# Performance work log

Hardware: AMD Instinct MI355X
Metric: run time of the kernel (lower is better)

## Reference

```python
import jax, jax.numpy as jnp
import numpy as np

B, QS, KS, E, H = 2, 2048, 2048, 2048, 16
D = E // H  # head_dim = 128
EPS = 1e-6


def setup_inputs() -> dict:
    key = jax.random.key(0)
    ks = jax.random.split(key, 11)
    scale_in = 1.0 / np.sqrt(E)  # lecun_normal fan_in = E
    scale_out = 1.0 / np.sqrt(E)  # fan_in for out proj = H*D = E
    return {
        "q": jax.random.normal(ks[0], (B, QS, E), jnp.float32),
        "kv": jax.random.normal(ks[1], (B, KS, E), jnp.float32),
        "q_pos": jax.random.normal(ks[2], (B, QS, E), jnp.float32),
        "kv_pos": jax.random.normal(ks[3], (B, KS, E), jnp.float32),
        "mask": jax.random.bernoulli(ks[4], 0.5, (B, QS, KS)),
        "wq": jax.random.normal(ks[5], (E, H, D), jnp.float32) * scale_in,
        "wk": jax.random.normal(ks[6], (E, H, D), jnp.float32) * scale_in,
        "wv": jax.random.normal(ks[7], (E, H, D), jnp.float32) * scale_in,
        "q_ln_scale": jnp.ones((D,), jnp.float32),
        "k_ln_scale": jnp.ones((D,), jnp.float32),
        "wo": jax.random.normal(ks[8], (H, D, E), jnp.float32) * scale_out,
    }


def _layernorm_no_bias(x, scale):
    # flax LayerNorm over last axis, use_bias=False, epsilon=1e-6
    mu = jnp.mean(x, axis=-1, keepdims=True)
    var = jnp.mean(jnp.square(x - mu), axis=-1, keepdims=True)
    return (x - mu) * jax.lax.rsqrt(var + EPS) * scale


def reference(q, kv, q_pos, kv_pos, mask, wq, wk, wv, q_ln_scale, k_ln_scale, wo):
    dtype = q.dtype
    qi = q + q_pos          # [b, qs, e]
    ki = kv + kv_pos        # [b, ks, e]
    vi = kv
    # QKV projections (DenseGeneral, no bias) -> [b, s, h, d]
    qh = jnp.einsum('bqe,ehd->bqhd', qi, wq)
    kh = jnp.einsum('bke,ehd->bkhd', ki, wk)
    vh = jnp.einsum('bke,ehd->bkhd', vi, wv)
    # normalize_qk: LayerNorm (no bias) on query/key over head_dim
    qh = _layernorm_no_bias(qh, q_ln_scale)
    kh = _layernorm_no_bias(kh, k_ln_scale)
    # scaled dot-product with float32 logits
    qh = qh / jnp.sqrt(jnp.asarray(D, dtype))
    logits = jnp.einsum('bqhd,bkhd->bhqk', qh, kh,
                        preferred_element_type=jnp.float32)
    big_neg = jnp.finfo(jnp.float32).min
    logits = jnp.where(mask[:, None, :, :], logits, big_neg)
    attn = jax.nn.softmax(logits, axis=-1).astype(dtype)  # [b,h,q,k]
    out = jnp.einsum('bhqk,bkhd->bqhd', attn, vh)
    # output projection (DenseGeneral over (h,d), no bias)
    return jnp.einsum('bqhd,hde->bqe', out, wo)
```

## Files before the change

### kernel.cpp

```cpp
#include <hip/hip_runtime.h>
#include <hip/hip_bf16.h>


typedef __attribute__((ext_vector_type(8))) __bf16 bf16x8;
typedef __attribute__((ext_vector_type(4))) float f32x4;
typedef __attribute__((ext_vector_type(16))) float f32x16;
typedef __attribute__((ext_vector_type(8))) unsigned short ushort8;
typedef __attribute__((ext_vector_type(4))) unsigned short ushort4v;
typedef __attribute__((ext_vector_type(4))) unsigned uint4v;
typedef __attribute__((ext_vector_type(4))) float float4v;

#define MFMA16(a, b, c) __builtin_amdgcn_mfma_f32_16x16x32_bf16((a), (b), (c), 0, 0, 0)
#define MFMA32(a, b, c) __builtin_amdgcn_mfma_f32_32x32x16_bf16((a), (b), (c), 0, 0, 0)

__device__ __forceinline__ unsigned short f2bf(float f) {
  unsigned u = __builtin_bit_cast(unsigned, f);
  u += 0x7fffu + ((u >> 16) & 1u);
  return (unsigned short)(u >> 16);
}

__device__ __forceinline__ unsigned pkbf(float lo, float hi) {
  unsigned d;
  asm("v_cvt_pk_bf16_f32 %0, %1, %2" : "=v"(d) : "v"(lo), "v"(hi));
  return d;
}

__device__ __forceinline__ float max3f(float a, float b, float c) {
  float d;
  asm("v_max3_f32 %0, %1, %2, %3" : "=v"(d) : "v"(a), "v"(b), "v"(c));
  return d;
}

__device__ __forceinline__ float exp2a(float x) {
  float d;
  asm("v_exp_f32 %0, %1" : "=v"(d) : "v"(x));
  return d;
}

__device__ __forceinline__ void gload_lds16(const void* g, void* l) {
  __builtin_amdgcn_global_load_lds(
      (const __attribute__((address_space(1))) void*)g,
      (__attribute__((address_space(3))) void*)l, 16, 0, 0);
}

__global__ __launch_bounds__(256) void k_prep(const float4v* __restrict__ q,
                                              const float4v* __restrict__ q_pos,
                                              const float4v* __restrict__ kv,
                                              const float4v* __restrict__ kv_pos,
                                              const int* __restrict__ mask,
                                              ushort4v* __restrict__ a_q,
                                              ushort4v* __restrict__ a_k,
                                              ushort4v* __restrict__ a_v,
                                              unsigned long long* __restrict__ mkb,
                                              const float* __restrict__ s0, const float* __restrict__ s1,
                                              const float* __restrict__ s2, const float* __restrict__ s3,
                                              unsigned short* __restrict__ d0, unsigned short* __restrict__ d1,
                                              unsigned short* __restrict__ d2, unsigned short* __restrict__ d3) {
  __shared__ float t[32][33];
  int bx = blockIdx.x, tid = threadIdx.x;
  if (bx < 8192) {
    int i = bx * 256 + tid;
    float4v a = q[i] + q_pos[i];
    ushort4v r;
    r[0] = f2bf(a[0]); r[1] = f2bf(a[1]); r[2] = f2bf(a[2]); r[3] = f2bf(a[3]);
    a_q[i] = r;
  } else if (bx < 16384) {
    int i = (bx - 8192) * 256 + tid;
    float4v a = kv[i];
    float4v s = a + kv_pos[i];
    ushort4v ra, rb;
    ra[0] = f2bf(s[0]); ra[1] = f2bf(s[1]); ra[2] = f2bf(s[2]); ra[3] = f2bf(s[3]);
    rb[0] = f2bf(a[0]); rb[1] = f2bf(a[1]); rb[2] = f2bf(a[2]); rb[3] = f2bf(a[3]);
    a_k[i] = ra; a_v[i] = rb;
  } else if (bx < 49152) {
    int i = (bx - 16384) * 256 + tid;
    unsigned long long b = __ballot(mask[i] != 0);
    if ((tid & 63) == 0) mkb[i >> 6] = b;
  } else {
    int idx = bx - 49152;
    int z = idx >> 12, rem = idx & 4095;
    int r0 = (rem >> 6) * 32, c0 = (rem & 63) * 32;
    const float* S; unsigned short* D;
    switch (z) {
      case 0: S = s0; D = d0; break;
      case 1: S = s1; D = d1; break;
      case 2: S = s2; D = d2; break;
      default: S = s3; D = d3; break;
    }
    int x = tid & 31, y = tid >> 5;
#pragma unroll
    for (int i = 0; i < 4; ++i) t[y + 8 * i][x] = S[(size_t)(r0 + y + 8 * i) * 2048 + c0 + x];
    __syncthreads();
#pragma unroll
    for (int i = 0; i < 4; ++i)
      D[(size_t)(c0 + y + 8 * i) * 2048 + r0 + x] = f2bf(t[x][y + 8 * i]);
  }
}

template <int MODE>
__global__ __launch_bounds__(512, 2) void k_gemm8(const unsigned short* __restrict__ A,
                                                  const unsigned short* __restrict__ Bt,
                                                  void* __restrict__ Cv,
                                                  const float* __restrict__ lnsc) {
  constexpr int K = 2048;
  constexpr int NT = 32;
  constexpr int BUF = 49152;
  __shared__ __attribute__((aligned(16))) char smem[3 * BUF];
  int tid = threadIdx.x;
  int lane = tid & 63, w = tid >> 6;
  int wr = w >> 2, wc = w & 3;
  int r15 = lane & 15, blk = lane >> 4;
  int L = blockIdx.y * gridDim.x + blockIdx.x;
  int xcd = L & 7, slot = L >> 3;
  int mt, nt;
  if constexpr (MODE == 4) { mt = xcd; nt = slot; }
  else { mt = xcd * 2 + (slot >> 4); nt = slot & 15; }
  int n0 = nt * 128, m0 = mt * 256;
  const unsigned short* Abase = A + (size_t)m0 * K;
  const unsigned short* Bbase = Bt + (size_t)n0 * K;
  f32x4 acc[8][2] = {};

  const unsigned short* ag[4]; int al[4];
  const unsigned short* bg[2]; int bl[2];
#pragma unroll
  for (int i = 0; i < 4; ++i) {
    int c = i * 512 + tid;
    int row = c >> 3, cc = c & 7;
    ag[i] = Abase + (size_t)row * K + ((cc ^ (row & 7)) * 8);
    al[i] = c * 16;
  }
#pragma unroll
  for (int i = 0; i < 2; ++i) {
    int c = i * 512 + tid;
    int row = c >> 3, cc = c & 7;
    bg[i] = Bbase + (size_t)row * K + ((cc ^ (row & 7)) * 8);
    bl[i] = 32768 + c * 16;
  }

  auto stage = [&](int t) {
    char* buf = smem + (t % 3) * BUF;
    int kt = t * 64;
#pragma unroll
    for (int i = 0; i < 4; ++i) gload_lds16(ag[i] + kt, buf + al[i]);
#pragma unroll
    for (int i = 0; i < 2; ++i) gload_lds16(bg[i] + kt, buf + bl[i]);
  };

  stage(0);
  stage(1);

  for (int t = 0; t < NT; ++t) {
    if (t + 2 < NT) {
      stage(t + 2);
      asm volatile("s_waitcnt vmcnt(12)" ::: "memory");
    } else if (t + 1 < NT) {
      asm volatile("s_waitcnt vmcnt(6)" ::: "memory");
    } else {
      asm volatile("s_waitcnt vmcnt(0)" ::: "memory");
    }
    __builtin_amdgcn_s_barrier();
    __builtin_amdgcn_sched_barrier(0);
    const unsigned short* sA = (const unsigned short*)(smem + (t % 3) * BUF);
    const unsigned short* sB = (const unsigned short*)(smem + (t % 3) * BUF + 32768);
#pragma unroll
    for (int kk = 0; kk < 2; ++kk) {
      bf16x8 av[8], bv[2];
#pragma unroll
      for (int i = 0; i < 8; ++i) {
        int row = wr * 128 + i * 16 + r15;
        av[i] = *(const bf16x8*)&sA[row * 64 + (((kk * 4 + blk) ^ (row & 7)) * 8)];
      }
#pragma unroll
      for (int j = 0; j < 2; ++j) {
        int row = wc * 32 + j * 16 + r15;
        bv[j] = *(const bf16x8*)&sB[row * 64 + (((kk * 4 + blk) ^ (row & 7)) * 8)];
      }
#pragma unroll
      for (int i = 0; i < 8; ++i)
#pragma unroll
        for (int j = 0; j < 2; ++j) acc[i][j] = MFMA16(av[i], bv[j], acc[i][j]);
    }
    asm volatile("s_waitcnt lgkmcnt(0)" ::: "memory");
    __builtin_amdgcn_s_barrier();
  }
  __syncthreads();

  if constexpr (MODE == 3) {
    float* C = (float*)Cv;
#pragma unroll
    for (int i = 0; i < 8; ++i)
#pragma unroll
      for (int r = 0; r < 4; ++r) {
        int rowl = wr * 128 + i * 16 + blk * 4 + r;
#pragma unroll
        for (int j = 0; j < 2; ++j) {
          int coll = wc * 32 + j * 16 + r15;
          C[(size_t)(m0 + rowl) * 2048 + n0 + coll] = acc[i][j][r];
        }
      }
  } else if constexpr (MODE == 4) {
    unsigned short* Vtp = (unsigned short*)Cv;
    int p15 = (r15 & 3) | ((r15 & 4) << 1) | ((r15 & 8) >> 1);
#pragma unroll
    for (int i = 0; i < 8; ++i)
#pragma unroll
      for (int r = 0; r < 4; ++r) {
        int rowg = m0 + wr * 128 + i * 16 + blk * 4 + r;
        int h = rowg >> 7, d = rowg & 127;
#pragma unroll
        for (int j = 0; j < 2; ++j) {
          int col = n0 + wc * 32 + j * 16;
          int b = col >> 11, s16 = col & 2047;
          Vtp[(((size_t)(b * 16 + h) * 128 + d) * 2048) + s16 + p15] = f2bf(acc[i][j][r]);
        }
      }
  } else {
    float* sSum = (float*)smem;
    float* sSq  = (float*)smem + 1024;
#pragma unroll
    for (int i = 0; i < 8; ++i)
#pragma unroll
      for (int r = 0; r < 4; ++r) {
        float v0 = acc[i][0][r], v1 = acc[i][1][r];
        float sm = v0 + v1, sq = v0 * v0 + v1 * v1;
        sm += __shfl_xor(sm, 1); sq += __shfl_xor(sq, 1);
        sm += __shfl_xor(sm, 2); sq += __shfl_xor(sq, 2);
        sm += __shfl_xor(sm, 4); sq += __shfl_xor(sq, 4);
        sm += __shfl_xor(sm, 8); sq += __shfl_xor(sq, 8);
        if (r15 == 0) {
          int rowl = wr * 128 + i * 16 + blk * 4 + r;
          sSum[wc * 256 + rowl] = sm;
          sSq[wc * 256 + rowl] = sq;
        }
      }
    __syncthreads();
    unsigned short* Hout = (unsigned short*)Cv;
    int h = nt;
#pragma unroll
    for (int i = 0; i < 8; ++i)
#pragma unroll
      for (int r = 0; r < 4; ++r) {
        int rowl = wr * 128 + i * 16 + blk * 4 + r;
        float sm = (sSum[rowl] + sSum[256 + rowl]) + (sSum[512 + rowl] + sSum[768 + rowl]);
        float sq = (sSq[rowl] + sSq[256 + rowl]) + (sSq[512 + rowl] + sSq[768 + rowl]);
        float mean = sm * 0.0078125f;
        float var = sq * 0.0078125f - mean * mean;
        float rstd = rsqrtf(var + 1e-6f);
        int rowg = m0 + rowl;
        int b = rowg >> 11, s = rowg & 2047;
        unsigned short* orow = Hout + (((size_t)b * 16 + h) * 2048 + s) * 128;
#pragma unroll
        for (int j = 0; j < 2; ++j) {
          int d = wc * 32 + j * 16 + r15;
          float v = acc[i][j][r];
          if constexpr (MODE == 1)
            v = (v - mean) * rstd * lnsc[d] * (0.08838834764831845f * 1.4426950408889634f);
          else
            v = (v - mean) * rstd * lnsc[d];
          orow[d] = f2bf(v);
        }
      }
  }
}

__global__ __launch_bounds__(256, 2) void k_attn(const unsigned short* __restrict__ Qh,
                                                 const unsigned short* __restrict__ Kh,
                                                 const unsigned short* __restrict__ Vtp,
                                                 const unsigned* __restrict__ maskb,
                                                 unsigned short* __restrict__ O) {
  __shared__ __attribute__((aligned(16))) char smem[65536];
  int tid = threadIdx.x, w = tid >> 6;
  int lane = tid & 63;
  int q31 = lane & 31, hi = lane >> 5;
  int L = blockIdx.y * 16 + blockIdx.x;
  int xcd = L & 7, slot = L >> 3;
  int bh = xcd * 4 + (slot >> 4);
  int qb = (slot & 15) * 128;
  int b = bh >> 4, h = bh & 15;
  size_t base = (size_t)bh * (2048 * 128);
  int qrow = qb + w * 32 + q31;

  bf16x8 qf[8];
  {
    const unsigned short* qp = Qh + base + (size_t)qrow * 128 + hi * 8;
#pragma unroll
    for (int wd = 0; wd < 8; ++wd) qf[wd] = *(const bf16x8*)(qp + wd * 16);
  }
  const unsigned* mrow = maskb + ((size_t)b * 2048 + qrow) * 64;

  const unsigned short* kgp[4];
  const unsigned short* vgp[4];
#pragma unroll
  for (int i = 0; i < 4; ++i) {
    int c = i * 256 + tid;
    int rr = c >> 4, cc = c & 15;
    kgp[i] = Kh + base + (size_t)rr * 128 + ((cc ^ (rr & 15)) * 8);
    int d = c >> 3, c8 = c & 7;
    vgp[i] = Vtp + base + (size_t)d * 2048 + ((c8 ^ (d & 7)) * 8);
  }

  f32x16 o[4] = {};
  float mv = -1e30f, ls = 0.f;

#pragma unroll
  for (int i = 0; i < 4; ++i) {
    int c = i * 256 + tid;
    gload_lds16(kgp[i], smem + c * 16);
    gload_lds16(vgp[i], smem + 16384 + c * 16);
  }
  __syncthreads();

  int cur = 0;
  for (int kc = 0; kc < 2048; kc += 64) {
    if (kc + 64 < 2048) {
      char* nb = smem + ((cur ^ 1) << 15);
#pragma unroll
      for (int i = 0; i < 4; ++i) {
        int c = i * 256 + tid;
        gload_lds16(kgp[i] + (size_t)(kc + 64) * 128, nb + c * 16);
        gload_lds16(vgp[i] + (kc + 64), nb + 16384 + c * 16);
      }
    }
    const unsigned short* sK = (const unsigned short*)(smem + (cur << 15));
    const unsigned short* sV = (const unsigned short*)(smem + (cur << 15) + 16384);

    unsigned mw0 = mrow[kc >> 5] >> (4 * hi);
    unsigned mw1 = mrow[(kc >> 5) + 1] >> (4 * hi);

    f32x16 st0 = {}, st1 = {};
    __builtin_amdgcn_s_setprio(1);
#pragma unroll
    for (int wd = 0; wd < 8; ++wd) {
      int ck = ((2 * wd + hi) ^ (q31 & 15)) * 8;
      bf16x8 k0 = *(const bf16x8*)&sK[q31 * 128 + ck];
      bf16x8 k1 = *(const bf16x8*)&sK[(32 + q31) * 128 + ck];
      st0 = MFMA32(k0, qf[wd], st0);
      st1 = MFMA32(k1, qf[wd], st1);
    }
    __builtin_amdgcn_s_setprio(0);

    float pvv[32];
#pragma unroll
    for (int r = 0; r < 16; ++r) {
      int bit = (r & 3) + 8 * (r >> 2);
      pvv[r] = ((mw0 >> bit) & 1u) ? st0[r] : -1e30f;
      pvv[16 + r] = ((mw1 >> bit) & 1u) ? st1[r] : -1e30f;
    }
    float c0 = max3f(pvv[0], pvv[1], pvv[2]);
    float c1 = max3f(pvv[3], pvv[4], pvv[5]);
    float c2 = max3f(pvv[6], pvv[7], pvv[8]);
    float c3 = max3f(pvv[9], pvv[10], pvv[11]);
    float c4 = max3f(pvv[12], pvv[13], pvv[14]);
    float c5 = max3f(pvv[15], pvv[16], pvv[17]);
    float c6 = max3f(pvv[18], pvv[19], pvv[20]);
    float c7 = max3f(pvv[21], pvv[22], pvv[23]);
    float c8 = max3f(pvv[24], pvv[25], pvv[26]);
    float c9 = max3f(pvv[27], pvv[28], pvv[29]);
    float ca = fmaxf(pvv[30], pvv[31]);
    float t0 = max3f(c0, c1, c2);
    float t1 = max3f(c3, c4, c5);
    float t2 = max3f(c6, c7, c8);
    float t3 = max3f(c9, ca, t0);
    float cmax = max3f(t1, t2, t3);
    cmax = fmaxf(cmax, __shfl_xor(cmax, 32));

    if (!__all(cmax - mv <= 11.5f)) {
      float mnew = fmaxf(mv, cmax);
      float fac = exp2a(mv - mnew);
      ls *= fac;
      float fr[16];
#pragma unroll
      for (int r = 0; r < 16; ++r) fr[r] = __shfl(fac, (r & 3) + 8 * (r >> 2) + 4 * hi);
#pragma unroll
      for (int dt = 0; dt < 4; ++dt)
#pragma unroll
        for (int r = 0; r < 16; ++r) o[dt][r] *= fr[r];
      mv = mnew;
    }

#pragma unroll
    for (int t = 0; t < 32; ++t) pvv[t] = exp2a(pvv[t] - mv);
    {
      float s0 = 0.f, s1 = 0.f, s2 = 0.f, s3 = 0.f;
#pragma unroll
      for (int t = 0; t < 8; ++t) {
        s0 += pvv[t]; s1 += pvv[8 + t]; s2 += pvv[16 + t]; s3 += pvv[24 + t];
      }
      ls += (s0 + s1) + (s2 + s3);
    }

    bf16x8 pa[4];
#pragma unroll
    for (int kw = 0; kw < 4; ++kw) {
      uint4v pw;
#pragma unroll
      for (int m = 0; m < 4; ++m) pw[m] = pkbf(pvv[8 * kw + 2 * m], pvv[8 * kw + 2 * m + 1]);
      pa[kw] = __builtin_bit_cast(bf16x8, pw);
    }

    __builtin_amdgcn_s_setprio(1);
#pragma unroll
    for (int dt = 0; dt < 4; ++dt) {
      int vrow = dt * 32 + q31;
#pragma unroll
      for (int kw = 0; kw < 4; ++kw) {
        int cv = ((2 * kw + hi) ^ (q31 & 7)) * 8;
        bf16x8 vf = *(const bf16x8*)&sV[vrow * 64 + cv];
        o[dt] = MFMA32(pa[kw], vf, o[dt]);
      }
    }
    __builtin_amdgcn_s_setprio(0);
    __syncthreads();
    cur ^= 1;
  }

  ls += __shfl_xor(ls, 32);
  float inv = 1.f / ls;
  float ir[16];
#pragma unroll
  for (int r = 0; r < 16; ++r) ir[r] = __shfl(inv, (r & 3) + 8 * (r >> 2) + 4 * hi);

  float* sO = (float*)smem;
#pragma unroll
  for (int pass = 0; pass < 2; ++pass) {
    __syncthreads();
    if ((w >> 1) == pass) {
      int wl = w & 1;
#pragma unroll
      for (int dt = 0; dt < 4; ++dt)
#pragma unroll
        for (int r = 0; r < 16; ++r) {
          int qrl = wl * 32 + (r & 3) + 8 * (r >> 2) + 4 * hi;
          sO[qrl * 132 + dt * 32 + q31] = o[dt][r] * ir[r];
        }
    }
    __syncthreads();
    {
      int row = tid >> 2, d0 = (tid & 3) * 32;
      int grow = qb + pass * 64 + row;
      unsigned short* op = O + (size_t)(b * 2048 + grow) * 2048 + h * 128 + d0;
#pragma unroll
      for (int g = 0; g < 4; ++g) {
        ushort8 pk;
#pragma unroll
        for (int e = 0; e < 8; ++e) pk[e] = f2bf(sO[row * 132 + d0 + g * 8 + e]);
        *(ushort8*)(op + g * 8) = pk;
      }
    }
  }
}

extern "C" void kernel_launch(void* const* d_in, const int* in_sizes, int n_in,
                              void* d_out, int out_size, void* d_ws, size_t ws_size,
                              hipStream_t stream) {
  const float* q      = (const float*)d_in[0];
  const float* kv     = (const float*)d_in[1];
  const float* q_pos  = (const float*)d_in[2];
  const float* kv_pos = (const float*)d_in[3];
  const int*   mask   = (const int*)d_in[4];
  const float* wq     = (const float*)d_in[5];
  const float* wk     = (const float*)d_in[6];
  const float* wv     = (const float*)d_in[7];
  const float* qls    = (const float*)d_in[8];
  const float* kls    = (const float*)d_in[9];
  const float* wo     = (const float*)d_in[10];

  char* ws = (char*)d_ws;
  const size_t SZ_ACT = (size_t)4096 * 2048 * 2;
  const size_t SZ_W   = (size_t)2048 * 2048 * 2;
  unsigned short* a_q = (unsigned short*)(ws);
  unsigned short* a_k = (unsigned short*)(ws + SZ_ACT);
  unsigned short* a_v = (unsigned short*)(ws + 2 * SZ_ACT);
  unsigned short* Qh  = (unsigned short*)(ws + 3 * SZ_ACT);
  unsigned short* Kh  = (unsigned short*)(ws + 4 * SZ_ACT);
  unsigned short* wqt = (unsigned short*)(ws + 6 * SZ_ACT);
  unsigned short* wkt = (unsigned short*)(ws + 6 * SZ_ACT + SZ_W);
  unsigned short* wvt = (unsigned short*)(ws + 6 * SZ_ACT + 2 * SZ_W);
  unsigned short* wot = (unsigned short*)(ws + 6 * SZ_ACT + 3 * SZ_W);
  unsigned*       mkb = (unsigned*)(ws + 6 * SZ_ACT + 4 * SZ_W);
  unsigned short* Ob  = a_q;
  unsigned short* Vtr = (unsigned short*)(ws + 5 * SZ_ACT);

  const size_t NEED = 6 * SZ_ACT + 4 * SZ_W + (size_t)2 * 2048 * 64 * 4;
  if (ws_size < NEED) return;

  k_prep<<<65536, 256, 0, stream>>>((const float4v*)q, (const float4v*)q_pos,
                                    (const float4v*)kv, (const float4v*)kv_pos, mask,
                                    (ushort4v*)a_q, (ushort4v*)a_k, (ushort4v*)a_v,
                                    (unsigned long long*)mkb,
                                    wq, wk, wv, wo, wqt, wkt, wvt, wot);

  k_gemm8<1><<<dim3(16, 16), 512, 0, stream>>>(a_q, wqt, Qh, qls);
  k_gemm8<2><<<dim3(16, 16), 512, 0, stream>>>(a_k, wkt, Kh, kls);
  k_gemm8<4><<<dim3(32, 8), 512, 0, stream>>>(wvt, a_v, Vtr, nullptr);

  k_attn<<<dim3(16, 32), 256, 0, stream>>>(Qh, Kh, Vtr, mkb, Ob);

  k_gemm8<3><<<dim3(16, 16), 512, 0, stream>>>(Ob, wot, d_out, nullptr);
}
```

Before: 314.4 us.

## Merge Q/K/V projection GEMMs into one launch and coarsen prep kernel

The three separate QKV projection GEMM launches become one 768-block kernel that picks its mode from the block index, so the three projections can overlap and fill the GPU instead of running as three 256-block waves. The prep kernel now handles two or four elements per thread for the elementwise and mask-packing parts, halving its grid. The setprio calls around the MFMA sections in attention are removed. The output projection gets its own specialised kernel. The risk is extra register pressure or divergence from runtime mode selection in the fused kernel.

Result: faster. 307.0 us (-2.4%).

```diff
diff --git a/kernel.cpp b/kernel.cpp
--- a/kernel.cpp
+++ b/kernel.cpp
@@ -58,26 +58,35 @@
                                               unsigned short* __restrict__ d2, unsigned short* __restrict__ d3) {
   __shared__ float t[32][33];
   int bx = blockIdx.x, tid = threadIdx.x;
-  if (bx < 8192) {
-    int i = bx * 256 + tid;
-    float4v a = q[i] + q_pos[i];
-    ushort4v r;
-    r[0] = f2bf(a[0]); r[1] = f2bf(a[1]); r[2] = f2bf(a[2]); r[3] = f2bf(a[3]);
-    a_q[i] = r;
+  if (bx < 4096) {
+#pragma unroll
+    for (int k = 0; k < 2; ++k) {
+      int i = bx * 256 + tid + k * 1048576;
+      float4v a = q[i] + q_pos[i];
+      ushort4v r;
+      r[0] = f2bf(a[0]); r[1] = f2bf(a[1]); r[2] = f2bf(a[2]); r[3] = f2bf(a[3]);
+      a_q[i] = r;
+    }
+  } else if (bx < 8192) {
+#pragma unroll
+    for (int k = 0; k < 2; ++k) {
+      int i = (bx - 4096) * 256 + tid + k * 1048576;
+      float4v a = kv[i];
+      float4v s = a + kv_pos[i];
+      ushort4v ra, rb;
+      ra[0] = f2bf(s[0]); ra[1] = f2bf(s[1]); ra[2] = f2bf(s[2]); ra[3] = f2bf(s[3]);
+      rb[0] = f2bf(a[0]); rb[1] = f2bf(a[1]); rb[2] = f2bf(a[2]); rb[3] = f2bf(a[3]);
+      a_k[i] = ra; a_v[i] = rb;
+    }
   } else if (bx < 16384) {
-    int i = (bx - 8192) * 256 + tid;
-    float4v a = kv[i];
-    float4v s = a + kv_pos[i];
-    ushort4v ra, rb;
-    ra[0] = f2bf(s[0]); ra[1] = f2bf(s[1]); ra[2] = f2bf(s[2]); ra[3] = f2bf(s[3]);
-    rb[0] = f2bf(a[0]); rb[1] = f2bf(a[1]); rb[2] = f2bf(a[2]); rb[3] = f2bf(a[3]);
-    a_k[i] = ra; a_v[i] = rb;
-  } else if (bx < 49152) {
-    int i = (bx - 16384) * 256 + tid;
-    unsigned long long b = __ballot(mask[i] != 0);
-    if ((tid & 63) == 0) mkb[i >> 6] = b;
+#pragma unroll
+    for (int k = 0; k < 4; ++k) {
+      int i = (bx - 8192) * 256 + tid + k * 2097152;
+      unsigned long long b = __ballot(mask[i] != 0);
+      if ((tid & 63) == 0) mkb[i >> 6] = b;
+    }
   } else {
-    int idx = bx - 49152;
+    int idx = bx - 16384;
     int z = idx >> 12, rem = idx & 4095;
     int r0 = (rem >> 6) * 32, c0 = (rem & 63) * 32;
     const float* S; unsigned short* D;
@@ -97,11 +106,17 @@
   }
 }
 
-template <int MODE>
-__global__ __launch_bounds__(512, 2) void k_gemm8(const unsigned short* __restrict__ A,
-                                                  const unsigned short* __restrict__ Bt,
-                                                  void* __restrict__ Cv,
-                                                  const float* __restrict__ lnsc) {
+__global__ __launch_bounds__(512, 2) void k_qkv(const unsigned short* __restrict__ a_q,
+                                                const unsigned short* __restrict__ wqt,
+                                                unsigned short* __restrict__ Qh,
+                                                const float* __restrict__ qls,
+                                                const unsigned short* __restrict__ a_k,
+                                                const unsigned short* __restrict__ wkt,
+                                                unsigned short* __restrict__ Kh,
+                                                const float* __restrict__ kls,
+                                                const unsigned short* __restrict__ wvt,
+                                                const unsigned short* __restrict__ a_v,
+                                                unsigned short* __restrict__ Vtp) {
   constexpr int K = 2048;
   constexpr int NT = 32;
   constexpr int BUF = 49152;
@@ -110,12 +125,15 @@
   int lane = tid & 63, w = tid >> 6;
   int wr = w >> 2, wc = w & 3;
   int r15 = lane & 15, blk = lane >> 4;
-  int L = blockIdx.y * gridDim.x + blockIdx.x;
+  int mode = blockIdx.x >> 8;
+  int L = blockIdx.x & 255;
   int xcd = L & 7, slot = L >> 3;
   int mt, nt;
-  if constexpr (MODE == 4) { mt = xcd; nt = slot; }
+  if (mode == 2) { mt = xcd; nt = slot; }
   else { mt = xcd * 2 + (slot >> 4); nt = slot & 15; }
   int n0 = nt * 128, m0 = mt * 256;
+  const unsigned short* A = (mode == 0) ? a_q : (mode == 1) ? a_k : wvt;
+  const unsigned short* Bt = (mode == 0) ? wqt : (mode == 1) ? wkt : a_v;
   const unsigned short* Abase = A + (size_t)m0 * K;
   const unsigned short* Bbase = Bt + (size_t)n0 * K;
   f32x4 acc[8][2] = {};
@@ -185,21 +203,7 @@
   }
   __syncthreads();
 
-  if constexpr (MODE == 3) {
-    float* C = (float*)Cv;
-#pragma unroll
-    for (int i = 0; i < 8; ++i)
-#pragma unroll
-      for (int r = 0; r < 4; ++r) {
-        int rowl = wr * 128 + i * 16 + blk * 4 + r;
-#pragma unroll
-        for (int j = 0; j < 2; ++j) {
-          int coll = wc * 32 + j * 16 + r15;
-          C[(size_t)(m0 + rowl) * 2048 + n0 + coll] = acc[i][j][r];
-        }
-      }
-  } else if constexpr (MODE == 4) {
-    unsigned short* Vtp = (unsigned short*)Cv;
+  if (mode == 2) {
     int p15 = (r15 & 3) | ((r15 & 4) << 1) | ((r15 & 8) >> 1);
 #pragma unroll
     for (int i = 0; i < 8; ++i)
@@ -234,7 +238,9 @@
         }
       }
     __syncthreads();
-    unsigned short* Hout = (unsigned short*)Cv;
+    unsigned short* Hout = (mode == 0) ? Qh : Kh;
+    const float* lnsc = (mode == 0) ? qls : kls;
+    float qmul = (mode == 0) ? (0.08838834764831845f * 1.4426950408889634f) : 1.0f;
     int h = nt;
 #pragma unroll
     for (int i = 0; i < 8; ++i)
@@ -253,14 +259,107 @@
         for (int j = 0; j < 2; ++j) {
           int d = wc * 32 + j * 16 + r15;
           float v = acc[i][j][r];
-          if constexpr (MODE == 1)
-            v = (v - mean) * rstd * lnsc[d] * (0.08838834764831845f * 1.4426950408889634f);
-          else
-            v = (v - mean) * rstd * lnsc[d];
+          v = (v - mean) * rstd * lnsc[d] * qmul;
           orow[d] = f2bf(v);
         }
       }
   }
+}
+
+__global__ __launch_bounds__(512, 2) void k_oproj(const unsigned short* __restrict__ A,
+                                                  const unsigned short* __restrict__ Bt,
+                                                  float* __restrict__ C) {
+  constexpr int K = 2048;
+  constexpr int NT = 32;
+  constexpr int BUF = 49152;
+  __shared__ __attribute__((aligned(16))) char smem[3 * BUF];
+  int tid = threadIdx.x;
+  int lane = tid & 63, w = tid >> 6;
+  int wr = w >> 2, wc = w & 3;
+  int r15 = lane & 15, blk = lane >> 4;
+  int L = blockIdx.y * gridDim.x + blockIdx.x;
+  int xcd = L & 7, slot = L >> 3;
+  int mt = xcd * 2 + (slot >> 4), nt = slot & 15;
+  int n0 = nt * 128, m0 = mt * 256;
+  const unsigned short* Abase = A + (size_t)m0 * K;
+  const unsigned short* Bbase = Bt + (size_t)n0 * K;
+  f32x4 acc[8][2] = {};
+
+  const unsigned short* ag[4]; int al[4];
+  const unsigned short* bg[2]; int bl[2];
+#pragma unroll
+  for (int i = 0; i < 4; ++i) {
+    int c = i * 512 + tid;
+    int row = c >> 3, cc = c & 7;
+    ag[i] = Abase + (size_t)row * K + ((cc ^ (row & 7)) * 8);
+    al[i] = c * 16;
+  }
+#pragma unroll
+  for (int i = 0; i < 2; ++i) {
+    int c = i * 512 + tid;
+    int row = c >> 3, cc = c & 7;
+    bg[i] = Bbase + (size_t)row * K + ((cc ^ (row & 7)) * 8);
+    bl[i] = 32768 + c * 16;
+  }
+
+  auto stage = [&](int t) {
+    char* buf = smem + (t % 3) * BUF;
+    int kt = t * 64;
+#pragma unroll
+    for (int i = 0; i < 4; ++i) gload_lds16(ag[i] + kt, buf + al[i]);
+#pragma unroll
+    for (int i = 0; i < 2; ++i) gload_lds16(bg[i] + kt, buf + bl[i]);
+  };
+
+  stage(0);
+  stage(1);
+
+  for (int t = 0; t < NT; ++t) {
+    if (t + 2 < NT) {
+      stage(t + 2);
+      asm volatile("s_waitcnt vmcnt(12)" ::: "memory");
+    } else if (t + 1 < NT) {
+      asm volatile("s_waitcnt vmcnt(6)" ::: "memory");
+    } else {
+      asm volatile("s_waitcnt vmcnt(0)" ::: "memory");
+    }
+    __builtin_amdgcn_s_barrier();
+    __builtin_amdgcn_sched_barrier(0);
+    const unsigned short* sA = (const unsigned short*)(smem + (t % 3) * BUF);
+    const unsigned short* sB = (const unsigned short*)(smem + (t % 3) * BUF + 32768);
+#pragma unroll
+    for (int kk = 0; kk < 2; ++kk) {
+      bf16x8 av[8], bv[2];
+#pragma unroll
+      for (int i = 0; i < 8; ++i) {
+        int row = wr * 128 + i * 16 + r15;
+        av[i] = *(const bf16x8*)&sA[row * 64 + (((kk * 4 + blk) ^ (row & 7)) * 8)];
+      }
+#pragma unroll
+      for (int j = 0; j < 2; ++j) {
+        int row = wc * 32 + j * 16 + r15;
+        bv[j] = *(const bf16x8*)&sB[row * 64 + (((kk * 4 + blk) ^ (row & 7)) * 8)];
+      }
+#pragma unroll
+      for (int i = 0; i < 8; ++i)
+#pragma unroll
+        for (int j = 0; j < 2; ++j) acc[i][j] = MFMA16(av[i], bv[j], acc[i][j]);
+    }
+    asm volatile("s_waitcnt lgkmcnt(0)" ::: "memory");
+    __builtin_amdgcn_s_barrier();
+  }
+
+#pragma unroll
+  for (int i = 0; i < 8; ++i)
+#pragma unroll
+    for (int r = 0; r < 4; ++r) {
+      int rowl = wr * 128 + i * 16 + blk * 4 + r;
+#pragma unroll
+      for (int j = 0; j < 2; ++j) {
+        int coll = wc * 32 + j * 16 + r15;
+        C[(size_t)(m0 + rowl) * 2048 + n0 + coll] = acc[i][j][r];
+      }
+    }
 }
 
 __global__ __launch_bounds__(256, 2) void k_attn(const unsigned short* __restrict__ Qh,
@@ -328,7 +427,6 @@
     unsigned mw1 = mrow[(kc >> 5) + 1] >> (4 * hi);
 
     f32x16 st0 = {}, st1 = {};
-    __builtin_amdgcn_s_setprio(1);
 #pragma unroll
     for (int wd = 0; wd < 8; ++wd) {
       int ck = ((2 * wd + hi) ^ (q31 & 15)) * 8;
@@ -337,7 +435,6 @@
       st0 = MFMA32(k0, qf[wd], st0);
       st1 = MFMA32(k1, qf[wd], st1);
     }
-    __builtin_amdgcn_s_setprio(0);
 
     float pvv[32];
 #pragma unroll
@@ -398,7 +495,6 @@
       pa[kw] = __builtin_bit_cast(bf16x8, pw);
     }
 
-    __builtin_amdgcn_s_setprio(1);
 #pragma unroll
     for (int dt = 0; dt < 4; ++dt) {
       int vrow = dt * 32 + q31;
@@ -409,7 +505,6 @@
         o[dt] = MFMA32(pa[kw], vf, o[dt]);
       }
     }
-    __builtin_amdgcn_s_setprio(0);
     __syncthreads();
     cur ^= 1;
   }
@@ -484,17 +579,15 @@
   const size_t NEED = 6 * SZ_ACT + 4 * SZ_W + (size_t)2 * 2048 * 64 * 4;
   if (ws_size < NEED) return;
 
-  k_prep<<<65536, 256, 0, stream>>>((const float4v*)q, (const float4v*)q_pos,
+  k_prep<<<32768, 256, 0, stream>>>((const float4v*)q, (const float4v*)q_pos,
                                     (const float4v*)kv, (const float4v*)kv_pos, mask,
                                     (ushort4v*)a_q, (ushort4v*)a_k, (ushort4v*)a_v,
                                     (unsigned long long*)mkb,
                                     wq, wk, wv, wo, wqt, wkt, wvt, wot);
 
-  k_gemm8<1><<<dim3(16, 16), 512, 0, stream>>>(a_q, wqt, Qh, qls);
-  k_gemm8<2><<<dim3(16, 16), 512, 0, stream>>>(a_k, wkt, Kh, kls);
-  k_gemm8<4><<<dim3(32, 8), 512, 0, stream>>>(wvt, a_v, Vtr, nullptr);
+  k_qkv<<<768, 512, 0, stream>>>(a_q, wqt, Qh, qls, a_k, wkt, Kh, kls, wvt, a_v, Vtr);
 
   k_attn<<<dim3(16, 32), 256, 0, stream>>>(Qh, Kh, Vtr, mkb, Ob);
 
-  k_gemm8<3><<<dim3(16, 16), 512, 0, stream>>>(Ob, wot, d_out, nullptr);
-}
+  k_oproj<<<dim3(16, 16), 512, 0, stream>>>(Ob, wot, (float*)d_out);
+}
```
